# Optimization experiments

Hardware: AMD Instinct MI355X
Metric: run time of the kernel (lower is better)

## Reference

```python
import jax, jax.numpy as jnp
import numpy as np
import math

B, S, D, H, DFF = 4, 2048, 1024, 16, 4096
DK = D // H
EPS = 1e-5


def setup_inputs() -> dict:
    key = jax.random.key(0)
    ks = jax.random.split(key, 12)
    sc = 0.02
    inp = {
        "x": jax.random.normal(ks[0], (B, S, D), dtype=jnp.float32),
        "mask": jnp.ones((B, 1, 1, S), dtype=jnp.int32),
        "Wq": jax.random.normal(ks[1], (D, D), jnp.float32) * sc,
        "bq": jnp.zeros((D,), jnp.float32),
        "Wk": jax.random.normal(ks[2], (D, D), jnp.float32) * sc,
        "bk": jnp.zeros((D,), jnp.float32),
        "Wv": jax.random.normal(ks[3], (D, D), jnp.float32) * sc,
        "bv": jnp.zeros((D,), jnp.float32),
        "Wo": jax.random.normal(ks[4], (D, D), jnp.float32) * sc,
        "bo": jnp.zeros((D,), jnp.float32),
        "ln1_g": jnp.ones((D,), jnp.float32),
        "ln1_b": jnp.zeros((D,), jnp.float32),
        "W1": jax.random.normal(ks[5], (D, DFF), jnp.float32) * sc,
        "b1": jnp.zeros((DFF,), jnp.float32),
        "W2": jax.random.normal(ks[6], (DFF, D), jnp.float32) * sc,
        "b2": jnp.zeros((D,), jnp.float32),
        "ln2_g": jnp.ones((D,), jnp.float32),
        "ln2_b": jnp.zeros((D,), jnp.float32),
    }
    return inp


def _layer_norm(x, g, b):
    m = jnp.mean(x, axis=-1, keepdims=True)
    v = jnp.mean(jnp.square(x - m), axis=-1, keepdims=True)
    return (x - m) * jax.lax.rsqrt(v + EPS) * g + b


def reference(x, mask, Wq, bq, Wk, bk, Wv, bv, Wo, bo,
              ln1_g, ln1_b, W1, b1, W2, b2, ln2_g, ln2_b):
    b_, s_, d_ = x.shape
    h_, dk_ = H, DK
    # --- pre-LN attention sublayer ---
    hidden = _layer_norm(x, ln1_g, ln1_b)
    q = (hidden @ Wq + bq).reshape(b_, s_, h_, dk_).transpose(0, 2, 1, 3)  # [B,H,S,dk]
    k = (hidden @ Wk + bk).reshape(b_, s_, h_, dk_).transpose(0, 2, 1, 3)  # [B,H,S,dk]
    # NOTE: original code passes value=key (the value projection is dead code),
    # so K is used both as keys and as values. Reproduced faithfully.
    scores = jnp.einsum("bhqd,bhkd->bhqk", q, k) / math.sqrt(dk_)  # [B,H,S,S]
    scores = jnp.where(mask == 0, jnp.float32(-1e9), scores)
    p_attn = jax.nn.softmax(scores, axis=-1)
    attn_out = jnp.einsum("bhqk,bhkd->bhqd", p_attn, k)  # values == k
    attn_out = attn_out.transpose(0, 2, 1, 3).reshape(b_, s_, d_)
    attn_out = attn_out @ Wo + bo
    x = x + attn_out  # residual (dropout is identity in eval)
    # --- pre-LN FFN sublayer ---
    hidden2 = _layer_norm(x, ln2_g, ln2_b)
    ff = jax.nn.gelu(hidden2 @ W1 + b1, approximate=False) @ W2 + b2
    return x + ff
```

## Files before the change

### kernel.cpp

```cpp
#include <hip/hip_runtime.h>
#include <hip/hip_bf16.h>
#include <math.h>

#define B_   4
#define S_   2048
#define D_   1024
#define H_   16
#define DK_  64
#define DFF_ 4096
#define M_   (B_*S_)

typedef __bf16 bf16;
typedef bf16 bf16x8 __attribute__((ext_vector_type(8)));
typedef bf16 bf16x4 __attribute__((ext_vector_type(4)));
typedef float f32x4 __attribute__((ext_vector_type(4)));

__device__ __forceinline__ void g2lds16(const void* g, void* l) {
  __builtin_amdgcn_global_load_lds(
      (__attribute__((address_space(1))) void*)(void*)g,
      (__attribute__((address_space(3))) void*)l, 16, 0, 0);
}

__device__ __forceinline__ void* swzp(char* base, int row, int byteofs) {
  return base + row * 128 + (byteofs ^ ((row & 7) << 4));
}

#define FENCE_ asm volatile("" ::: "memory")
#define BARR_  do { FENCE_; __builtin_amdgcn_s_barrier(); FENCE_; } while (0)
#define VMW4_  asm volatile("s_waitcnt vmcnt(4)" ::: "memory")
#define VMW0_  asm volatile("s_waitcnt vmcnt(0)" ::: "memory")
#define LGW_   do { asm volatile("s_waitcnt lgkmcnt(0)" ::: "memory"); \
                    __builtin_amdgcn_sched_barrier(0); } while (0)

__global__ void tcast_all(const float* __restrict__ Wq, const float* __restrict__ Wk,
                          const float* __restrict__ Wo, const float* __restrict__ W1,
                          const float* __restrict__ W2,
                          bf16* __restrict__ WqkT, bf16* __restrict__ WoT,
                          bf16* __restrict__ W1T, bf16* __restrict__ W2T) {
  __shared__ float t[32][33];
  int bid = blockIdx.x;
  const float* src; bf16* dst; int K, N, bx, by;
  if (bid < 1024)      { src = Wq; dst = WqkT;            K = 1024; N = 1024; bx = bid & 31;  by = bid >> 5; }
  else if (bid < 2048) { bid -= 1024; src = Wk; dst = WqkT + 1024 * 1024; K = 1024; N = 1024; bx = bid & 31;  by = bid >> 5; }
  else if (bid < 3072) { bid -= 2048; src = Wo; dst = WoT; K = 1024; N = 1024; bx = bid & 31;  by = bid >> 5; }
  else if (bid < 7168) { bid -= 3072; src = W1; dst = W1T; K = 1024; N = 4096; bx = bid & 127; by = bid >> 7; }
  else                 { bid -= 7168; src = W2; dst = W2T; K = 4096; N = 1024; bx = bid & 31;  by = bid >> 5; }
  int n0 = bx * 32, k0 = by * 32;
  int tx = threadIdx.x, ty = threadIdx.y;
#pragma unroll
  for (int i = 0; i < 4; ++i)
    t[ty + i*8][tx] = src[(size_t)(k0 + ty + i*8) * N + n0 + tx];
  __syncthreads();
#pragma unroll
  for (int i = 0; i < 4; ++i)
    dst[(size_t)(n0 + ty + i*8) * K + k0 + tx] = (bf16)t[tx][ty + i*8];
}

__global__ __launch_bounds__(256)
void ktrans(const bf16* __restrict__ Kt, bf16* __restrict__ KT) {
  __shared__ bf16 t[64][72];
  const int bh = blockIdx.y, s0 = blockIdx.x * 64, tid = threadIdx.x;
  const bf16* src = Kt + (size_t)bh * S_ * DK_;
  bf16* dst = KT + (size_t)bh * DK_ * S_;
#pragma unroll
  for (int i = 0; i < 2; ++i) {
    int c = tid * 2 + i;
    int r = c >> 3, col = (c & 7) * 8;
    *(bf16x8*)&t[r][col] = *(const bf16x8*)&src[(size_t)(s0 + r) * 64 + col];
  }
  __syncthreads();
  const int d = tid >> 2, sc = (tid & 3) * 16;
  bf16x8 v0, v1;
#pragma unroll
  for (int j = 0; j < 8; ++j) { v0[j] = t[sc + j][d]; v1[j] = t[sc + 8 + j][d]; }
  *(bf16x8*)&dst[(size_t)d * S_ + s0 + sc] = v0;
  *(bf16x8*)&dst[(size_t)d * S_ + s0 + sc + 8] = v1;
}

__global__ __launch_bounds__(256)
void ln_fwd(const float* __restrict__ x, const float* __restrict__ g,
            const float* __restrict__ be, bf16* __restrict__ out) {
  int row = blockIdx.x, tid = threadIdx.x;
  const float4 v = *(const float4*)&x[(size_t)row * D_ + tid * 4];
  float s = v.x + v.y + v.z + v.w;
  float q = v.x*v.x + v.y*v.y + v.z*v.z + v.w*v.w;
#pragma unroll
  for (int d = 32; d; d >>= 1) { s += __shfl_down(s, d); q += __shfl_down(q, d); }
  __shared__ float red[8];
  int wave = tid >> 6, lane = tid & 63;
  if (lane == 0) { red[wave*2] = s; red[wave*2+1] = q; }
  __syncthreads();
  float ts = red[0] + red[2] + red[4] + red[6];
  float tq = red[1] + red[3] + red[5] + red[7];
  float mean = ts * (1.0f / D_);
  float var  = tq * (1.0f / D_) - mean * mean;
  float rstd = rsqrtf(var + 1e-5f);
  const float4 gg = *(const float4*)&g[tid * 4];
  const float4 bb = *(const float4*)&be[tid * 4];
  bf16x4 ov;
  ov[0] = (bf16)((v.x - mean) * rstd * gg.x + bb.x);
  ov[1] = (bf16)((v.y - mean) * rstd * gg.y + bb.y);
  ov[2] = (bf16)((v.z - mean) * rstd * gg.z + bb.z);
  ov[3] = (bf16)((v.w - mean) * rstd * gg.w + bb.w);
  *(bf16x4*)&out[(size_t)row * D_ + tid * 4] = ov;
}

template <int EPI, int KK>
__global__ __launch_bounds__(512, 2)
void gemm8p(const bf16* __restrict__ A, const bf16* __restrict__ Bt, int N,
            const float* __restrict__ bias, const float* __restrict__ bias2,
            const float* __restrict__ resid, float scale,
            float* __restrict__ outf, bf16* __restrict__ outb,
            bf16* __restrict__ outb2) {
  constexpr int NT = KK / 64;
  __shared__ __align__(16) bf16 Ab[2][256 * 64];
  __shared__ __align__(16) bf16 Bb[2][256 * 64];
  const int tid = threadIdx.x, wave = tid >> 6, lane = tid & 63;
  const int wr = wave >> 2, wc = wave & 3;
  const int l15 = lane & 15, q4 = lane >> 4;

  const int gx = gridDim.x, nwg = gx * gridDim.y;
  int wg = blockIdx.y * gx + blockIdx.x;
  wg = (wg & 7) * (nwg >> 3) + (wg >> 3);
  const long arow = (long)(wg / gx) * 256;
  const long bcol = (long)(wg % gx) * 256;

  const int srow  = lane >> 3;
  const int sslot = (lane & 7) ^ srow;
  const bf16* gA = A  + (size_t)(arow + wave * 16 + srow) * KK + sslot * 8;
  const bf16* gB = Bt + (size_t)(bcol + wave * 16 + srow) * KK + sslot * 8;

  char* const ab0 = (char*)&Ab[0][0];
  char* const ab1 = (char*)&Ab[1][0];
  char* const bb0 = (char*)&Bb[0][0];
  char* const bb1 = (char*)&Bb[1][0];
  const int aoff0 = (wr * 128 + l15) * 128;
  const int boff0 = (wc * 64 + l15) * 128;
  const int sw    = (l15 & 7) << 4;
  const int kq0   = (q4 * 16) ^ sw;
  const int kq1   = (64 + q4 * 16) ^ sw;

  f32x4 acc[8][4] = {};
  bf16x8 af[4][2], bq[4][2];

#define STG(dst, gsrc, half, kt) do {                                        \
    long kc_ = (long)(((kt) < NT) ? (kt) : (NT - 1)) * 64;                   \
    g2lds16((gsrc) + (long)((half) * 128) * KK + kc_,                        \
            &(dst)[((half) * 128 + wave * 16) * 64]);                        \
    g2lds16((gsrc) + (long)((half) * 128 + 8) * KK + kc_,                    \
            &(dst)[((half) * 128 + wave * 16 + 8) * 64]);                    \
  } while (0)

#define RDA(base, half) do {                                                 \
    _Pragma("unroll")                                                        \
    for (int m_ = 0; m_ < 4; ++m_) {                                         \
      af[m_][0] = *(const bf16x8*)((base) + aoff0 + ((half)*4+m_)*2048 + kq0);\
      af[m_][1] = *(const bf16x8*)((base) + aoff0 + ((half)*4+m_)*2048 + kq1);\
    } } while (0)

#define RDB(base, nh) do {                                                   \
    _Pragma("unroll")                                                        \
    for (int n_ = 0; n_ < 2; ++n_) {                                         \
      bq[(nh)*2+n_][0] = *(const bf16x8*)((base) + boff0 + ((nh)*2+n_)*2048 + kq0);\
      bq[(nh)*2+n_][1] = *(const bf16x8*)((base) + boff0 + ((nh)*2+n_)*2048 + kq1);\
    } } while (0)

#define QUAD(mh, nh) do {                                                    \
    __builtin_amdgcn_s_setprio(1);                                          \
    _Pragma("unroll")                                                        \
    for (int ks_ = 0; ks_ < 2; ++ks_)                                        \
      _Pragma("unroll")                                                      \
      for (int m_ = 0; m_ < 4; ++m_)                                         \
        _Pragma("unroll")                                                    \
        for (int n_ = 0; n_ < 2; ++n_)                                       \
          acc[(mh)*4+m_][(nh)*2+n_] = __builtin_amdgcn_mfma_f32_16x16x32_bf16(\
              af[m_][ks_], bq[(nh)*2+n_][ks_], acc[(mh)*4+m_][(nh)*2+n_],    \
              0, 0, 0);                                                      \
    __builtin_amdgcn_s_setprio(0);                                          \
  } while (0)

  STG(Bb[0], gB, 0, 0); STG(Bb[0], gB, 1, 0);
  STG(Ab[0], gA, 0, 0); STG(Ab[0], gA, 1, 0);
  STG(Bb[1], gB, 0, 1); STG(Bb[1], gB, 1, 1);

  for (int it = 0; it < NT / 2; ++it) {
    const int t = it * 2;
    VMW4_; BARR_;
    RDA(ab0, 0); RDB(bb0, 0);
    STG(Ab[1], gA, 0, t + 1);
    LGW_; QUAD(0, 0); BARR_;
    RDB(bb0, 1);
    STG(Ab[1], gA, 1, t + 1);
    LGW_; QUAD(0, 1); BARR_;
    RDA(ab0, 1);
    STG(Bb[0], gB, 0, t + 2);
    LGW_; QUAD(1, 0); BARR_;
    STG(Bb[0], gB, 1, t + 2);
    QUAD(1, 1); BARR_;
    VMW4_; BARR_;
    RDA(ab1, 0); RDB(bb1, 0);
    STG(Ab[0], gA, 0, t + 2);
    LGW_; QUAD(0, 0); BARR_;
    RDB(bb1, 1);
    STG(Ab[0], gA, 1, t + 2);
    LGW_; QUAD(0, 1); BARR_;
    RDA(ab1, 1);
    STG(Bb[1], gB, 0, t + 3);
    LGW_; QUAD(1, 0); BARR_;
    STG(Bb[1], gB, 1, t + 3);
    QUAD(1, 1); BARR_;
  }
  VMW0_;

#pragma unroll
  for (int mi = 0; mi < 8; ++mi) {
#pragma unroll
    for (int ni = 0; ni < 4; ++ni) {
#pragma unroll
      for (int j = 0; j < 4; ++j) {
        long row = arow + wr * 128 + mi * 16 + q4 * 4 + j;
        long col = bcol + wc * 64 + ni * 16 + l15;
        float v = acc[mi][ni][j];
        if constexpr (EPI == 0) {
          int bb = (int)(row >> 11), ss = (int)(row & 2047);
          int hh = (int)(col >> 6) & 15, dd = (int)(col & 63);
          size_t idx = (((size_t)(bb * H_ + hh)) * S_ + ss) * DK_ + dd;
          if (col < 1024) outb[idx]  = (bf16)((v + bias[col]) * scale);
          else            outb2[idx] = (bf16)(v + bias2[col - 1024]);
        } else if constexpr (EPI == 1) {
          size_t idx = (size_t)row * N + col;
          outf[idx] = v + bias[col] + resid[idx];
        } else {
          size_t idx = (size_t)row * N + col;
          float tt = v + bias[col];
          outb[idx] = (bf16)(0.5f * tt * (1.0f + erff(tt * 0.70710678118654752f)));
        }
      }
    }
  }
#undef STG
#undef RDA
#undef RDB
#undef QUAD
}

__global__ __launch_bounds__(256)
void attn_fwd(const bf16* __restrict__ Q, const bf16* __restrict__ Kk,
              const bf16* __restrict__ KT, const int* __restrict__ mask,
              bf16* __restrict__ O) {
  __shared__ __align__(16) char Kl[2][64 * 128];
  __shared__ __align__(16) char Vl[2][64 * 128];
  __shared__ __align__(16) char Pl[4][16 * 128];

  const int tid = threadIdx.x, wave = tid >> 6, lane = tid & 63;
  const int bh = blockIdx.y, b = bh >> 4, h = bh & 15;
  const int q0 = blockIdx.x * 64;
  const int l15 = lane & 15, q4 = lane >> 4;

  const bf16* Qp = Q  + (size_t)bh * S_ * DK_;
  const bf16* Kp = Kk + (size_t)bh * S_ * DK_;
  const bf16* Tp = KT + (size_t)bh * DK_ * S_;

  const int qrow = q0 + wave * 16 + l15;
  const bf16x8 qf0 = *(const bf16x8*)&Qp[(size_t)qrow * 64 + q4 * 8];
  const bf16x8 qf1 = *(const bf16x8*)&Qp[(size_t)qrow * 64 + 32 + q4 * 8];

  int lz = 0;
  for (int i = tid; i < S_; i += 256) lz |= (mask[b * S_ + i] == 0);
  const bool anyz = __syncthreads_or(lz) != 0;

  const int c0 = tid * 2, c1 = tid * 2 + 1;
  const int sr0 = c0 >> 3, sb0 = c0 & 7;
  const int sr1 = c1 >> 3, sb1 = c1 & 7;

  int poff[16];
#pragma unroll
  for (int nt = 0; nt < 4; ++nt)
#pragma unroll
    for (int j = 0; j < 4; ++j) {
      int r = q4 * 4 + j;
      poff[nt * 4 + j] = r * 128 + ((((nt * 16 + l15) * 2)) ^ ((r & 7) << 4));
    }

  bf16x8 onesv;
#pragma unroll
  for (int i = 0; i < 8; ++i) onesv[i] = (bf16)1.0f;

  f32x4 o[4] = {};
  f32x4 ol = {};
  float m_r[4];
#pragma unroll
  for (int j = 0; j < 4; ++j) m_r[j] = -__builtin_inff();

  bf16x8 a0 = *(const bf16x8*)&Kp[(size_t)sr0 * 64 + sb0 * 8];
  bf16x8 a1 = *(const bf16x8*)&Kp[(size_t)sr1 * 64 + sb1 * 8];
  bf16x8 t0 = *(const bf16x8*)&Tp[(size_t)sr0 * S_ + sb0 * 8];
  bf16x8 t1 = *(const bf16x8*)&Tp[(size_t)sr1 * S_ + sb1 * 8];
  *(bf16x8*)swzp(Kl[0], sr0, sb0 * 16) = a0;
  *(bf16x8*)swzp(Kl[0], sr1, sb1 * 16) = a1;
  *(bf16x8*)swzp(Vl[0], sr0, sb0 * 16) = t0;
  *(bf16x8*)swzp(Vl[0], sr1, sb1 * 16) = t1;
  int cur = 0;

  for (int k0 = 0; k0 < S_; k0 += 64) {
    __syncthreads();

    const int nk = k0 + 64;
    if (nk < S_) {
      a0 = *(const bf16x8*)&Kp[(size_t)(nk + sr0) * 64 + sb0 * 8];
      a1 = *(const bf16x8*)&Kp[(size_t)(nk + sr1) * 64 + sb1 * 8];
      t0 = *(const bf16x8*)&Tp[(size_t)sr0 * S_ + nk + sb0 * 8];
      t1 = *(const bf16x8*)&Tp[(size_t)sr1 * S_ + nk + sb1 * 8];
    }

    f32x4 s[4];
#pragma unroll
    for (int nt = 0; nt < 4; ++nt) {
      bf16x8 kf0 = *(const bf16x8*)swzp(Kl[cur], nt * 16 + l15, q4 * 16);
      bf16x8 kf1 = *(const bf16x8*)swzp(Kl[cur], nt * 16 + l15, 64 + q4 * 16);
      f32x4 z = {};
      z     = __builtin_amdgcn_mfma_f32_16x16x32_bf16(qf0, kf0, z, 0, 0, 0);
      s[nt] = __builtin_amdgcn_mfma_f32_16x16x32_bf16(qf1, kf1, z, 0, 0, 0);
    }
    if (anyz) {
#pragma unroll
      for (int nt = 0; nt < 4; ++nt) {
        int m2 = mask[b * S_ + k0 + nt * 16 + l15];
        if (m2 == 0) {
#pragma unroll
          for (int j = 0; j < 4; ++j) s[nt][j] = -1e9f;
        }
      }
    }

    float tm[4];
#pragma unroll
    for (int j = 0; j < 4; ++j)
      tm[j] = fmaxf(fmaxf(s[0][j], s[1][j]), fmaxf(s[2][j], s[3][j]));
    bool ok = true;
#pragma unroll
    for (int j = 0; j < 4; ++j) ok = ok && (tm[j] <= m_r[j] + 8.0f);
    if (!__all(ok)) {
#pragma unroll
      for (int d = 1; d < 16; d <<= 1)
#pragma unroll
        for (int j = 0; j < 4; ++j)
          tm[j] = fmaxf(tm[j], __shfl_xor(tm[j], d));
#pragma unroll
      for (int j = 0; j < 4; ++j) {
        float mn = fmaxf(m_r[j], tm[j]);
        float sf = __builtin_amdgcn_exp2f(m_r[j] - mn);
        m_r[j] = mn;
        ol[j] *= sf;
#pragma unroll
        for (int nf = 0; nf < 4; ++nf) o[nf][j] *= sf;
      }
    }

#pragma unroll
    for (int nt = 0; nt < 4; ++nt)
#pragma unroll
      for (int j = 0; j < 4; ++j)
        *(bf16*)(&Pl[wave][0] + poff[nt * 4 + j]) =
            (bf16)__builtin_amdgcn_exp2f(s[nt][j] - m_r[j]);

    const bf16x8 pf0 = *(const bf16x8*)swzp(Pl[wave], l15, q4 * 16);
    const bf16x8 pf1 = *(const bf16x8*)swzp(Pl[wave], l15, 64 + q4 * 16);

    ol = __builtin_amdgcn_mfma_f32_16x16x32_bf16(pf0, onesv, ol, 0, 0, 0);
    ol = __builtin_amdgcn_mfma_f32_16x16x32_bf16(pf1, onesv, ol, 0, 0, 0);

#pragma unroll
    for (int nf = 0; nf < 4; ++nf) {
      bf16x8 vf0 = *(const bf16x8*)swzp(Vl[cur], nf * 16 + l15, q4 * 16);
      bf16x8 vf1 = *(const bf16x8*)swzp(Vl[cur], nf * 16 + l15, 64 + q4 * 16);
      o[nf] = __builtin_amdgcn_mfma_f32_16x16x32_bf16(pf0, vf0, o[nf], 0, 0, 0);
      o[nf] = __builtin_amdgcn_mfma_f32_16x16x32_bf16(pf1, vf1, o[nf], 0, 0, 0);
    }

    if (nk < S_) {
      *(bf16x8*)swzp(Kl[cur ^ 1], sr0, sb0 * 16) = a0;
      *(bf16x8*)swzp(Kl[cur ^ 1], sr1, sb1 * 16) = a1;
      *(bf16x8*)swzp(Vl[cur ^ 1], sr0, sb0 * 16) = t0;
      *(bf16x8*)swzp(Vl[cur ^ 1], sr1, sb1 * 16) = t1;
    }
    cur ^= 1;
  }

#pragma unroll
  for (int nf = 0; nf < 4; ++nf)
#pragma unroll
    for (int j = 0; j < 4; ++j) {
      int row = q0 + wave * 16 + q4 * 4 + j;
      int col = h * 64 + nf * 16 + l15;
      O[((size_t)b * S_ + row) * D_ + col] = (bf16)(o[nf][j] / ol[j]);
    }
}

extern "C" void kernel_launch(void* const* d_in, const int* in_sizes, int n_in,
                              void* d_out, int out_size, void* d_ws, size_t ws_size,
                              hipStream_t stream) {
  const float* x    = (const float*)d_in[0];
  const int*   mask = (const int*)d_in[1];
  const float* Wq   = (const float*)d_in[2];
  const float* bq   = (const float*)d_in[3];
  const float* Wk   = (const float*)d_in[4];
  const float* bk   = (const float*)d_in[5];
  const float* Wo   = (const float*)d_in[8];
  const float* bo   = (const float*)d_in[9];
  const float* ln1g = (const float*)d_in[10];
  const float* ln1b = (const float*)d_in[11];
  const float* W1   = (const float*)d_in[12];
  const float* b1   = (const float*)d_in[13];
  const float* W2   = (const float*)d_in[14];
  const float* b2   = (const float*)d_in[15];
  const float* ln2g = (const float*)d_in[16];
  const float* ln2b = (const float*)d_in[17];
  float* out = (float*)d_out;

  char* w = (char*)d_ws;
  auto alloc = [&](size_t bytes) {
    void* p = (void*)w;
    w += (bytes + 255) & ~(size_t)255;
    return p;
  };
  bf16* xln  = (bf16*)alloc((size_t)M_ * D_ * 2);
  bf16* WqkT = (bf16*)alloc((size_t)2 * D_ * D_ * 2);
  bf16* WoT  = (bf16*)alloc((size_t)D_ * D_ * 2);
  bf16* W1T  = (bf16*)alloc((size_t)D_ * DFF_ * 2);
  bf16* W2T  = (bf16*)alloc((size_t)D_ * DFF_ * 2);
  bf16* Qt   = (bf16*)alloc((size_t)M_ * D_ * 2);
  bf16* Kt   = (bf16*)alloc((size_t)M_ * D_ * 2);
  bf16* KTt  = (bf16*)alloc((size_t)M_ * D_ * 2);
  bf16* attn = (bf16*)alloc((size_t)M_ * D_ * 2);
  float* x2  = (float*)alloc((size_t)M_ * D_ * 4);
  bf16* h2   = (bf16*)alloc((size_t)M_ * D_ * 2);
  bf16* act  = (bf16*)alloc((size_t)M_ * DFF_ * 2);

  tcast_all<<<11264, dim3(32, 8), 0, stream>>>(Wq, Wk, Wo, W1, W2,
                                               WqkT, WoT, W1T, W2T);

  ln_fwd<<<M_, 256, 0, stream>>>(x, ln1g, ln1b, xln);

  gemm8p<0, 1024><<<dim3(8, 32), 512, 0, stream>>>(
      xln, WqkT, 2048, bq, bk, nullptr,
      0.125f * 1.4426950408889634f, nullptr, Qt, Kt);

  ktrans<<<dim3(S_ / 64, B_ * H_), 256, 0, stream>>>(Kt, KTt);

  attn_fwd<<<dim3(S_ / 64, B_ * H_), 256, 0, stream>>>(Qt, Kt, KTt, mask, attn);

  gemm8p<1, 1024><<<dim3(4, 32), 512, 0, stream>>>(
      attn, WoT, 1024, bo, nullptr, x, 1.0f, x2, nullptr, nullptr);

  ln_fwd<<<M_, 256, 0, stream>>>(x2, ln2g, ln2b, h2);

  gemm8p<2, 1024><<<dim3(16, 32), 512, 0, stream>>>(
      h2, W1T, 4096, b1, nullptr, nullptr, 1.0f, nullptr, act, nullptr);

  gemm8p<1, 4096><<<dim3(4, 32), 512, 0, stream>>>(
      act, W2T, 1024, b2, nullptr, x2, 1.0f, out, nullptr, nullptr);
}
```

Baseline: 604.5 us.

## Process two query subtiles per wave in attention and reorder GEMM tile mapping

The attention kernel now gives each wave 32 query rows as two 16-row subtiles, so a block covers 128 queries and every K/V tile staged in LDS feeds twice as much MFMA work. The grid is halved, which cuts redundant K/V global loads and LDS staging per query. The cost is more registers for the extra accumulators and per-row softmax state, and fewer blocks available to fill the GPU. Separately, the GEMM workgroup-to-tile mapping now walks row tiles first within each column, changing which tiles run together and how they share the cache.

```diff
diff --git a/kernel.cpp b/kernel.cpp
--- a/kernel.cpp
+++ b/kernel.cpp
@@ -119,11 +119,11 @@
   const int wr = wave >> 2, wc = wave & 3;
   const int l15 = lane & 15, q4 = lane >> 4;
 
-  const int gx = gridDim.x, nwg = gx * gridDim.y;
+  const int gx = gridDim.x, rows = gridDim.y, nwg = gx * rows;
   int wg = blockIdx.y * gx + blockIdx.x;
   wg = (wg & 7) * (nwg >> 3) + (wg >> 3);
-  const long arow = (long)(wg / gx) * 256;
-  const long bcol = (long)(wg % gx) * 256;
+  const long arow = (long)(wg % rows) * 256;
+  const long bcol = (long)(wg / rows) * 256;
 
   const int srow  = lane >> 3;
   const int sslot = (lane & 7) ^ srow;
@@ -250,20 +250,23 @@
               bf16* __restrict__ O) {
   __shared__ __align__(16) char Kl[2][64 * 128];
   __shared__ __align__(16) char Vl[2][64 * 128];
-  __shared__ __align__(16) char Pl[4][16 * 128];
+  __shared__ __align__(16) char Pl[4][2][16 * 128];
 
   const int tid = threadIdx.x, wave = tid >> 6, lane = tid & 63;
   const int bh = blockIdx.y, b = bh >> 4, h = bh & 15;
-  const int q0 = blockIdx.x * 64;
+  const int q0 = blockIdx.x * 128;
   const int l15 = lane & 15, q4 = lane >> 4;
 
   const bf16* Qp = Q  + (size_t)bh * S_ * DK_;
   const bf16* Kp = Kk + (size_t)bh * S_ * DK_;
   const bf16* Tp = KT + (size_t)bh * DK_ * S_;
 
-  const int qrow = q0 + wave * 16 + l15;
-  const bf16x8 qf0 = *(const bf16x8*)&Qp[(size_t)qrow * 64 + q4 * 8];
-  const bf16x8 qf1 = *(const bf16x8*)&Qp[(size_t)qrow * 64 + 32 + q4 * 8];
+  const int qrA = q0 + wave * 32 + l15;
+  const int qrB = qrA + 16;
+  const bf16x8 qfA0 = *(const bf16x8*)&Qp[(size_t)qrA * 64 + q4 * 8];
+  const bf16x8 qfA1 = *(const bf16x8*)&Qp[(size_t)qrA * 64 + 32 + q4 * 8];
+  const bf16x8 qfB0 = *(const bf16x8*)&Qp[(size_t)qrB * 64 + q4 * 8];
+  const bf16x8 qfB1 = *(const bf16x8*)&Qp[(size_t)qrB * 64 + 32 + q4 * 8];
 
   int lz = 0;
   for (int i = tid; i < S_; i += 256) lz |= (mask[b * S_ + i] == 0);
@@ -286,11 +289,13 @@
 #pragma unroll
   for (int i = 0; i < 8; ++i) onesv[i] = (bf16)1.0f;
 
-  f32x4 o[4] = {};
-  f32x4 ol = {};
-  float m_r[4];
-#pragma unroll
-  for (int j = 0; j < 4; ++j) m_r[j] = -__builtin_inff();
+  f32x4 o[2][4] = {};
+  f32x4 ol[2] = {};
+  float m_r[2][4];
+#pragma unroll
+  for (int st = 0; st < 2; ++st)
+#pragma unroll
+    for (int j = 0; j < 4; ++j) m_r[st][j] = -__builtin_inff();
 
   bf16x8 a0 = *(const bf16x8*)&Kp[(size_t)sr0 * 64 + sb0 * 8];
   bf16x8 a1 = *(const bf16x8*)&Kp[(size_t)sr1 * 64 + sb1 * 8];
@@ -313,14 +318,16 @@
       t1 = *(const bf16x8*)&Tp[(size_t)sr1 * S_ + nk + sb1 * 8];
     }
 
-    f32x4 s[4];
+    f32x4 s[2][4];
 #pragma unroll
     for (int nt = 0; nt < 4; ++nt) {
       bf16x8 kf0 = *(const bf16x8*)swzp(Kl[cur], nt * 16 + l15, q4 * 16);
       bf16x8 kf1 = *(const bf16x8*)swzp(Kl[cur], nt * 16 + l15, 64 + q4 * 16);
-      f32x4 z = {};
-      z     = __builtin_amdgcn_mfma_f32_16x16x32_bf16(qf0, kf0, z, 0, 0, 0);
-      s[nt] = __builtin_amdgcn_mfma_f32_16x16x32_bf16(qf1, kf1, z, 0, 0, 0);
+      f32x4 zA = {}, zB = {};
+      zA = __builtin_amdgcn_mfma_f32_16x16x32_bf16(qfA0, kf0, zA, 0, 0, 0);
+      s[0][nt] = __builtin_amdgcn_mfma_f32_16x16x32_bf16(qfA1, kf1, zA, 0, 0, 0);
+      zB = __builtin_amdgcn_mfma_f32_16x16x32_bf16(qfB0, kf0, zB, 0, 0, 0);
+      s[1][nt] = __builtin_amdgcn_mfma_f32_16x16x32_bf16(qfB1, kf1, zB, 0, 0, 0);
     }
     if (anyz) {
 #pragma unroll
@@ -328,54 +335,69 @@
         int m2 = mask[b * S_ + k0 + nt * 16 + l15];
         if (m2 == 0) {
 #pragma unroll
-          for (int j = 0; j < 4; ++j) s[nt][j] = -1e9f;
+          for (int j = 0; j < 4; ++j) { s[0][nt][j] = -1e9f; s[1][nt][j] = -1e9f; }
         }
       }
     }
 
-    float tm[4];
-#pragma unroll
-    for (int j = 0; j < 4; ++j)
-      tm[j] = fmaxf(fmaxf(s[0][j], s[1][j]), fmaxf(s[2][j], s[3][j]));
+    float tm[2][4];
     bool ok = true;
 #pragma unroll
-    for (int j = 0; j < 4; ++j) ok = ok && (tm[j] <= m_r[j] + 8.0f);
+    for (int st = 0; st < 2; ++st)
+#pragma unroll
+      for (int j = 0; j < 4; ++j) {
+        tm[st][j] = fmaxf(fmaxf(s[st][0][j], s[st][1][j]),
+                          fmaxf(s[st][2][j], s[st][3][j]));
+        ok = ok && (tm[st][j] <= m_r[st][j] + 8.0f);
+      }
     if (!__all(ok)) {
 #pragma unroll
       for (int d = 1; d < 16; d <<= 1)
 #pragma unroll
+        for (int st = 0; st < 2; ++st)
+#pragma unroll
+          for (int j = 0; j < 4; ++j)
+            tm[st][j] = fmaxf(tm[st][j], __shfl_xor(tm[st][j], d));
+#pragma unroll
+      for (int st = 0; st < 2; ++st)
+#pragma unroll
+        for (int j = 0; j < 4; ++j) {
+          float mn = fmaxf(m_r[st][j], tm[st][j]);
+          float sf = __builtin_amdgcn_exp2f(m_r[st][j] - mn);
+          m_r[st][j] = mn;
+          ol[st][j] *= sf;
+#pragma unroll
+          for (int nf = 0; nf < 4; ++nf) o[st][nf][j] *= sf;
+        }
+    }
+
+#pragma unroll
+    for (int st = 0; st < 2; ++st)
+#pragma unroll
+      for (int nt = 0; nt < 4; ++nt)
+#pragma unroll
         for (int j = 0; j < 4; ++j)
-          tm[j] = fmaxf(tm[j], __shfl_xor(tm[j], d));
-#pragma unroll
-      for (int j = 0; j < 4; ++j) {
-        float mn = fmaxf(m_r[j], tm[j]);
-        float sf = __builtin_amdgcn_exp2f(m_r[j] - mn);
-        m_r[j] = mn;
-        ol[j] *= sf;
-#pragma unroll
-        for (int nf = 0; nf < 4; ++nf) o[nf][j] *= sf;
-      }
-    }
-
-#pragma unroll
-    for (int nt = 0; nt < 4; ++nt)
-#pragma unroll
-      for (int j = 0; j < 4; ++j)
-        *(bf16*)(&Pl[wave][0] + poff[nt * 4 + j]) =
-            (bf16)__builtin_amdgcn_exp2f(s[nt][j] - m_r[j]);
-
-    const bf16x8 pf0 = *(const bf16x8*)swzp(Pl[wave], l15, q4 * 16);
-    const bf16x8 pf1 = *(const bf16x8*)swzp(Pl[wave], l15, 64 + q4 * 16);
-
-    ol = __builtin_amdgcn_mfma_f32_16x16x32_bf16(pf0, onesv, ol, 0, 0, 0);
-    ol = __builtin_amdgcn_mfma_f32_16x16x32_bf16(pf1, onesv, ol, 0, 0, 0);
+          *(bf16*)(&Pl[wave][st][0] + poff[nt * 4 + j]) =
+              (bf16)__builtin_amdgcn_exp2f(s[st][nt][j] - m_r[st][j]);
+
+    const bf16x8 pfA0 = *(const bf16x8*)swzp(&Pl[wave][0][0], l15, q4 * 16);
+    const bf16x8 pfA1 = *(const bf16x8*)swzp(&Pl[wave][0][0], l15, 64 + q4 * 16);
+    const bf16x8 pfB0 = *(const bf16x8*)swzp(&Pl[wave][1][0], l15, q4 * 16);
+    const bf16x8 pfB1 = *(const bf16x8*)swzp(&Pl[wave][1][0], l15, 64 + q4 * 16);
+
+    ol[0] = __builtin_amdgcn_mfma_f32_16x16x32_bf16(pfA0, onesv, ol[0], 0, 0, 0);
+    ol[0] = __builtin_amdgcn_mfma_f32_16x16x32_bf16(pfA1, onesv, ol[0], 0, 0, 0);
+    ol[1] = __builtin_amdgcn_mfma_f32_16x16x32_bf16(pfB0, onesv, ol[1], 0, 0, 0);
+    ol[1] = __builtin_amdgcn_mfma_f32_16x16x32_bf16(pfB1, onesv, ol[1], 0, 0, 0);
 
 #pragma unroll
     for (int nf = 0; nf < 4; ++nf) {
       bf16x8 vf0 = *(const bf16x8*)swzp(Vl[cur], nf * 16 + l15, q4 * 16);
       bf16x8 vf1 = *(const bf16x8*)swzp(Vl[cur], nf * 16 + l15, 64 + q4 * 16);
-      o[nf] = __builtin_amdgcn_mfma_f32_16x16x32_bf16(pf0, vf0, o[nf], 0, 0, 0);
-      o[nf] = __builtin_amdgcn_mfma_f32_16x16x32_bf16(pf1, vf1, o[nf], 0, 0, 0);
+      o[0][nf] = __builtin_amdgcn_mfma_f32_16x16x32_bf16(pfA0, vf0, o[0][nf], 0, 0, 0);
+      o[0][nf] = __builtin_amdgcn_mfma_f32_16x16x32_bf16(pfA1, vf1, o[0][nf], 0, 0, 0);
+      o[1][nf] = __builtin_amdgcn_mfma_f32_16x16x32_bf16(pfB0, vf0, o[1][nf], 0, 0, 0);
+      o[1][nf] = __builtin_amdgcn_mfma_f32_16x16x32_bf16(pfB1, vf1, o[1][nf], 0, 0, 0);
     }
 
     if (nk < S_) {
@@ -388,13 +410,15 @@
   }
 
 #pragma unroll
-  for (int nf = 0; nf < 4; ++nf)
-#pragma unroll
-    for (int j = 0; j < 4; ++j) {
-      int row = q0 + wave * 16 + q4 * 4 + j;
-      int col = h * 64 + nf * 16 + l15;
-      O[((size_t)b * S_ + row) * D_ + col] = (bf16)(o[nf][j] / ol[j]);
-    }
+  for (int st = 0; st < 2; ++st)
+#pragma unroll
+    for (int nf = 0; nf < 4; ++nf)
+#pragma unroll
+      for (int j = 0; j < 4; ++j) {
+        int row = q0 + wave * 32 + st * 16 + q4 * 4 + j;
+        int col = h * 64 + nf * 16 + l15;
+        O[((size_t)b * S_ + row) * D_ + col] = (bf16)(o[st][nf][j] / ol[st][j]);
+      }
 }
 
 extern "C" void kernel_launch(void* const* d_in, const int* in_sizes, int n_in,
@@ -448,7 +472,7 @@
 
   ktrans<<<dim3(S_ / 64, B_ * H_), 256, 0, stream>>>(Kt, KTt);
 
-  attn_fwd<<<dim3(S_ / 64, B_ * H_), 256, 0, stream>>>(Qt, Kt, KTt, mask, attn);
+  attn_fwd<<<dim3(S_ / 128, B_ * H_), 256, 0, stream>>>(Qt, Kt, KTt, mask, attn);
 
   gemm8p<1, 1024><<<dim3(4, 32), 512, 0, stream>>>(
       attn, WoT, 1024, bo, nullptr, x, 1.0f, x2, nullptr, nullptr);
```

New measurement: 716.4 us. 18.5% more time.
